# Performance work log

Hardware: AMD Instinct MI355X
Metric: run time of the kernel (lower is better)

Reference implementation:

```python
import jax, jax.numpy as jnp
import numpy as np

K = 64        # top-k from init_kwargs
TAU = 1.0     # temperature at step=0: tau_start*(1-0) + tau_end*0


def setup_inputs() -> dict:
    key = jax.random.key(0)
    k1, k2 = jax.random.split(key)
    B, N = 2048, 8192
    logits = jax.random.normal(k1, (B, N), dtype=jnp.float32)
    # gumbels = -log(Exp(1)) == standard Gumbel noise
    gumbel_noise = jax.random.gumbel(k2, (B, N), dtype=jnp.float32)
    return {"logits": logits, "gumbel_noise": gumbel_noise}


def reference(logits, gumbel_noise):
    # training path of GumbelTopK (step=0 -> tau=TAU, hard=True)
    g = (logits + gumbel_noise) / TAU                       # [B, N]
    order = jnp.argsort(-g, axis=-1)                        # descending sort order
    sorted_g = jnp.take_along_axis(g, order, axis=-1)
    cumsum = jnp.cumsum(jax.nn.softmax(sorted_g, axis=-1), axis=-1)
    mask = (cumsum <= K).astype(sorted_g.dtype)             # NB: faithful to source (<= k)
    sorted_y = mask * jax.nn.softmax(sorted_g / TAU, axis=-1)
    # scatter back to original positions == gather by inverse permutation
    inv = jnp.argsort(order, axis=-1)
    y = jnp.take_along_axis(sorted_y, inv, axis=-1)         # [B, N]
    # hard straight-through: one-hot-k of y
    k = min(K, y.shape[-1])
    _, idx = jax.lax.top_k(y, k)                            # [B, k]
    rows = jnp.arange(y.shape[0])[:, None]
    y_hard = jnp.zeros_like(y).at[rows, idx].set(1.0)
    return jax.lax.stop_gradient(y_hard - y) + y
```

## Files before the change

kernel.cpp:

```cpp
#include <hip/hip_runtime.h>

constexpr int N = 8192;
constexpr int K = 64;
constexpr int THREADS = 256;
constexpr int EPT = N / THREADS;
constexpr int HIST_BINS = 2048;

__device__ __forceinline__ unsigned orderable(float f) {
    unsigned x = __float_as_uint(f);
    return (x & 0x80000000u) ? ~x : (x | 0x80000000u);
}

__global__ __launch_bounds__(THREADS)
void gumbel_topk_onehot(const float* __restrict__ logits,
                        const float* __restrict__ noise,
                        float* __restrict__ out)
{
    __shared__ unsigned u_sh[N];
    __shared__ unsigned hist[HIST_BINS];
    __shared__ unsigned part[THREADS];
    __shared__ unsigned sel_prefix, sel_kth, sel_cnt;

    const int tid = threadIdx.x;
    const long long row = blockIdx.x;
    const float4* lrow = (const float4*)(logits + row * (long long)N);
    const float4* nrow = (const float4*)(noise  + row * (long long)N);

#pragma unroll
    for (int i = 0; i < EPT / 4; ++i) {
        int idx = tid + i * THREADS;
        float4 a = lrow[idx];
        float4 b = nrow[idx];
        u_sh[4 * idx + 0] = orderable(a.x + b.x);
        u_sh[4 * idx + 1] = orderable(a.y + b.y);
        u_sh[4 * idx + 2] = orderable(a.z + b.z);
        u_sh[4 * idx + 3] = orderable(a.w + b.w);
    }

    unsigned prefix = 0;
    unsigned kth = K;

#pragma unroll
    for (int r = 0; r < 3; ++r) {
        const int shift = (r == 0) ? 21 : (r == 1) ? 10 : 0;
        const int bits  = (r == 2) ? 10 : 11;
        const unsigned nb = 1u << bits;

        __syncthreads();
        for (int i = tid; i < HIST_BINS; i += THREADS) hist[i] = 0;
        __syncthreads();

        for (int i = tid; i < N; i += THREADS) {
            unsigned u = u_sh[i];
            bool match = (r == 0) ? true : ((u >> (shift + bits)) == prefix);
            if (match) atomicAdd(&hist[(u >> shift) & (nb - 1u)], 1u);
        }
        __syncthreads();

        const int bpt = nb / THREADS;
        unsigned p = 0;
#pragma unroll
        for (int j = 0; j < 8; ++j)
            if (j < bpt) p += hist[tid * bpt + j];
        part[tid] = p;
        __syncthreads();

        for (int off = 1; off < THREADS; off <<= 1) {
            unsigned v = (tid + off < THREADS) ? part[tid + off] : 0u;
            __syncthreads();
            part[tid] += v;
            __syncthreads();
        }

        unsigned snext = (tid + 1 < THREADS) ? part[tid + 1] : 0u;
        if (part[tid] >= kth && snext < kth) {
            unsigned cum = snext;
            for (int j = bpt - 1; j >= 0; --j) {
                unsigned c = hist[tid * bpt + j];
                if (cum + c >= kth) {
                    sel_prefix = (prefix << bits) | (unsigned)(tid * bpt + j);
                    sel_kth = kth - cum;
                    sel_cnt = c;
                    break;
                }
                cum += c;
            }
        }
        __syncthreads();
        prefix = sel_prefix;
        kth = sel_kth;
    }

    const unsigned T = prefix;
    const unsigned take_eq = kth;
    const unsigned c_eq = sel_cnt;
    const bool fastpath = (take_eq == c_eq);

    float4* orow = (float4*)(out + row * (long long)N);
#pragma unroll
    for (int i = 0; i < EPT / 4; ++i) {
        int idx = tid + i * THREADS;
        unsigned u0 = u_sh[4 * idx + 0];
        unsigned u1 = u_sh[4 * idx + 1];
        unsigned u2 = u_sh[4 * idx + 2];
        unsigned u3 = u_sh[4 * idx + 3];
        float4 o;
        o.x = (u0 > T || (fastpath && u0 == T)) ? 1.0f : 0.0f;
        o.y = (u1 > T || (fastpath && u1 == T)) ? 1.0f : 0.0f;
        o.z = (u2 > T || (fastpath && u2 == T)) ? 1.0f : 0.0f;
        o.w = (u3 > T || (fastpath && u3 == T)) ? 1.0f : 0.0f;
        orow[idx] = o;
    }

    if (!fastpath) {
        __syncthreads();
        if (tid == 0) {
            unsigned c = 0;
            float* orowf = out + row * (long long)N;
            for (int i = 0; i < N; ++i) {
                if (u_sh[i] == T) {
                    orowf[i] = 1.0f;
                    if (++c == take_eq) break;
                }
            }
        }
    }
}

extern "C" void kernel_launch(void* const* d_in, const int* in_sizes, int n_in,
                              void* d_out, int out_size, void* d_ws, size_t ws_size,
                              hipStream_t stream) {
    const float* logits = (const float*)d_in[0];
    const float* noise  = (const float*)d_in[1];
    float* out = (float*)d_out;
    const int rows = in_sizes[0] / N;
    gumbel_topk_onehot<<<rows, THREADS, 0, stream>>>(logits, noise, out);
}
```

Measured before the change: 185.6 us.

## Keep row keys in registers and radix-select over a compacted candidate list

Each thread now keeps its 32 keys in registers instead of staging the whole 8192-element row in shared memory. Passes two and three of the radix select build their histograms from a compacted candidate buffer of the first-pass bin, not by rescanning all N keys. The block-wide Hillis-Steele scan with many barriers is replaced by wave shuffle reductions, and launch bounds request 4 blocks per CU. In exchange the kernel uses more registers, the candidate buffer has a capacity fallback, and the rare tie path recomputes keys from global memory.

```diff
diff --git a/kernel.cpp b/kernel.cpp
--- a/kernel.cpp
+++ b/kernel.cpp
@@ -3,128 +3,185 @@
 constexpr int N = 8192;
 constexpr int K = 64;
 constexpr int THREADS = 256;
+constexpr int WAVES = THREADS / 64;
 constexpr int EPT = N / THREADS;
-constexpr int HIST_BINS = 2048;
+constexpr int VEC = EPT / 4;
+constexpr int CAP = 3072;
 
 __device__ __forceinline__ unsigned orderable(float f) {
     unsigned x = __float_as_uint(f);
     return (x & 0x80000000u) ? ~x : (x | 0x80000000u);
 }
 
-__global__ __launch_bounds__(THREADS)
+__global__ __launch_bounds__(THREADS, 4)
 void gumbel_topk_onehot(const float* __restrict__ logits,
                         const float* __restrict__ noise,
                         float* __restrict__ out)
 {
-    __shared__ unsigned u_sh[N];
-    __shared__ unsigned hist[HIST_BINS];
-    __shared__ unsigned part[THREADS];
-    __shared__ unsigned sel_prefix, sel_kth, sel_cnt;
+    __shared__ unsigned hist[2048];
+    __shared__ unsigned cand[CAP];
+    __shared__ unsigned wavesum[WAVES];
+    __shared__ unsigned ccount;
+    __shared__ unsigned sel_bin, sel_kth, sel_cnt;
 
-    const int tid = threadIdx.x;
+    const int tid  = threadIdx.x;
+    const int lane = tid & 63;
+    const int wave = tid >> 6;
     const long long row = blockIdx.x;
+
     const float4* lrow = (const float4*)(logits + row * (long long)N);
     const float4* nrow = (const float4*)(noise  + row * (long long)N);
 
+    unsigned key[EPT];
 #pragma unroll
-    for (int i = 0; i < EPT / 4; ++i) {
+    for (int i = 0; i < VEC; ++i) {
         int idx = tid + i * THREADS;
         float4 a = lrow[idx];
         float4 b = nrow[idx];
-        u_sh[4 * idx + 0] = orderable(a.x + b.x);
-        u_sh[4 * idx + 1] = orderable(a.y + b.y);
-        u_sh[4 * idx + 2] = orderable(a.z + b.z);
-        u_sh[4 * idx + 3] = orderable(a.w + b.w);
+        key[4*i+0] = orderable(a.x + b.x);
+        key[4*i+1] = orderable(a.y + b.y);
+        key[4*i+2] = orderable(a.z + b.z);
+        key[4*i+3] = orderable(a.w + b.w);
     }
 
-    unsigned prefix = 0;
+    {
+        uint4 z = make_uint4(0,0,0,0);
+        for (int i = tid; i < 512; i += THREADS) ((uint4*)hist)[i] = z;
+    }
+    if (tid == 0) ccount = 0;
+    __syncthreads();
+#pragma unroll
+    for (int e = 0; e < EPT; ++e)
+        atomicAdd(&hist[key[e] >> 21], 1u);
+    __syncthreads();
+
     unsigned kth = K;
 
-#pragma unroll
-    for (int r = 0; r < 3; ++r) {
-        const int shift = (r == 0) ? 21 : (r == 1) ? 10 : 0;
-        const int bits  = (r == 2) ? 10 : 11;
-        const unsigned nb = 1u << bits;
-
-        __syncthreads();
-        for (int i = tid; i < HIST_BINS; i += THREADS) hist[i] = 0;
-        __syncthreads();
-
-        for (int i = tid; i < N; i += THREADS) {
-            unsigned u = u_sh[i];
-            bool match = (r == 0) ? true : ((u >> (shift + bits)) == prefix);
-            if (match) atomicAdd(&hist[(u >> shift) & (nb - 1u)], 1u);
-        }
-        __syncthreads();
-
-        const int bpt = nb / THREADS;
-        unsigned p = 0;
-#pragma unroll
-        for (int j = 0; j < 8; ++j)
-            if (j < bpt) p += hist[tid * bpt + j];
-        part[tid] = p;
-        __syncthreads();
-
-        for (int off = 1; off < THREADS; off <<= 1) {
-            unsigned v = (tid + off < THREADS) ? part[tid + off] : 0u;
-            __syncthreads();
-            part[tid] += v;
-            __syncthreads();
-        }
-
-        unsigned snext = (tid + 1 < THREADS) ? part[tid + 1] : 0u;
-        if (part[tid] >= kth && snext < kth) {
-            unsigned cum = snext;
-            for (int j = bpt - 1; j >= 0; --j) {
-                unsigned c = hist[tid * bpt + j];
-                if (cum + c >= kth) {
-                    sel_prefix = (prefix << bits) | (unsigned)(tid * bpt + j);
-                    sel_kth = kth - cum;
-                    sel_cnt = c;
-                    break;
-                }
-                cum += c;
-            }
-        }
-        __syncthreads();
-        prefix = sel_prefix;
-        kth = sel_kth;
+#define SELECT_BIN(BPT)                                                      \
+    {                                                                        \
+        unsigned p = 0;                                                      \
+        _Pragma("unroll")                                                    \
+        for (int j = 0; j < (BPT); ++j) p += hist[tid * (BPT) + j];          \
+        unsigned s = p;                                                      \
+        _Pragma("unroll")                                                    \
+        for (int off = 1; off < 64; off <<= 1) {                             \
+            unsigned v = __shfl_down(s, off);                                \
+            if (lane + off < 64) s += v;                                     \
+        }                                                                    \
+        if (lane == 0) wavesum[wave] = s;                                    \
+        __syncthreads();                                                     \
+        unsigned S = s;                                                      \
+        _Pragma("unroll")                                                    \
+        for (int w = 0; w < WAVES; ++w) if (w > wave) S += wavesum[w];       \
+        unsigned Snext = S - p;                                              \
+        if (S >= kth && Snext < kth) {                                       \
+            unsigned cum = Snext;                                            \
+            for (int j = (BPT) - 1; j >= 0; --j) {                           \
+                unsigned c = hist[tid * (BPT) + j];                          \
+                if (cum + c >= kth) {                                        \
+                    sel_bin = (unsigned)(tid * (BPT) + j);                   \
+                    sel_kth = kth - cum;                                     \
+                    sel_cnt = c;                                             \
+                    break;                                                   \
+                }                                                            \
+                cum += c;                                                    \
+            }                                                                \
+        }                                                                    \
+        __syncthreads();                                                     \
     }
 
-    const unsigned T = prefix;
-    const unsigned take_eq = kth;
-    const unsigned c_eq = sel_cnt;
-    const bool fastpath = (take_eq == c_eq);
+    SELECT_BIN(8)
+    const unsigned b1   = sel_bin;
+    const unsigned cnt1 = sel_cnt;
+    kth = sel_kth;
+    __syncthreads();
+
+    const bool use_cand = (cnt1 <= (unsigned)CAP);
+#pragma unroll
+    for (int e = 0; e < EPT; ++e) {
+        if ((key[e] >> 21) == b1) {
+            unsigned pos = atomicAdd(&ccount, 1u);
+            if (pos < (unsigned)CAP) cand[pos] = key[e] & 0x1FFFFFu;
+        }
+    }
+
+    __syncthreads();
+    {
+        uint4 z = make_uint4(0,0,0,0);
+        for (int i = tid; i < 512; i += THREADS) ((uint4*)hist)[i] = z;
+    }
+    __syncthreads();
+    if (use_cand) {
+        for (int i = tid; i < (int)cnt1; i += THREADS)
+            atomicAdd(&hist[cand[i] >> 10], 1u);
+    } else {
+#pragma unroll
+        for (int e = 0; e < EPT; ++e)
+            if ((key[e] >> 21) == b1)
+                atomicAdd(&hist[(key[e] >> 10) & 0x7FFu], 1u);
+    }
+    __syncthreads();
+
+    SELECT_BIN(8)
+    const unsigned b2 = sel_bin;
+    kth = sel_kth;
+    __syncthreads();
+
+    {
+        uint4 z = make_uint4(0,0,0,0);
+        for (int i = tid; i < 256; i += THREADS) ((uint4*)hist)[i] = z;
+    }
+    __syncthreads();
+    if (use_cand) {
+        for (int i = tid; i < (int)cnt1; i += THREADS) {
+            unsigned cv = cand[i];
+            if ((cv >> 10) == b2) atomicAdd(&hist[cv & 0x3FFu], 1u);
+        }
+    } else {
+        const unsigned pfx = (b1 << 11) | b2;
+#pragma unroll
+        for (int e = 0; e < EPT; ++e)
+            if ((key[e] >> 10) == pfx)
+                atomicAdd(&hist[key[e] & 0x3FFu], 1u);
+    }
+    __syncthreads();
+
+    SELECT_BIN(4)
+    const unsigned b3      = sel_bin;
+    const unsigned take_eq = sel_kth;
+    const unsigned c_eq    = sel_cnt;
+
+    const unsigned T = (b1 << 21) | (b2 << 10) | b3;
+    const bool fast = (take_eq == c_eq);
 
     float4* orow = (float4*)(out + row * (long long)N);
 #pragma unroll
-    for (int i = 0; i < EPT / 4; ++i) {
+    for (int i = 0; i < VEC; ++i) {
         int idx = tid + i * THREADS;
-        unsigned u0 = u_sh[4 * idx + 0];
-        unsigned u1 = u_sh[4 * idx + 1];
-        unsigned u2 = u_sh[4 * idx + 2];
-        unsigned u3 = u_sh[4 * idx + 3];
         float4 o;
-        o.x = (u0 > T || (fastpath && u0 == T)) ? 1.0f : 0.0f;
-        o.y = (u1 > T || (fastpath && u1 == T)) ? 1.0f : 0.0f;
-        o.z = (u2 > T || (fastpath && u2 == T)) ? 1.0f : 0.0f;
-        o.w = (u3 > T || (fastpath && u3 == T)) ? 1.0f : 0.0f;
+        o.x = (key[4*i+0] > T || (fast && key[4*i+0] == T)) ? 1.0f : 0.0f;
+        o.y = (key[4*i+1] > T || (fast && key[4*i+1] == T)) ? 1.0f : 0.0f;
+        o.z = (key[4*i+2] > T || (fast && key[4*i+2] == T)) ? 1.0f : 0.0f;
+        o.w = (key[4*i+3] > T || (fast && key[4*i+3] == T)) ? 1.0f : 0.0f;
         orow[idx] = o;
     }
 
-    if (!fastpath) {
+    if (!fast) {
         __syncthreads();
         if (tid == 0) {
+            const float* lf = logits + row * (long long)N;
+            const float* nf = noise  + row * (long long)N;
+            float* of = out + row * (long long)N;
             unsigned c = 0;
-            float* orowf = out + row * (long long)N;
             for (int i = 0; i < N; ++i) {
-                if (u_sh[i] == T) {
-                    orowf[i] = 1.0f;
+                if (orderable(lf[i] + nf[i]) == T) {
+                    of[i] = 1.0f;
                     if (++c == take_eq) break;
                 }
             }
         }
     }
+#undef SELECT_BIN
 }
 
 extern "C" void kernel_launch(void* const* d_in, const int* in_sizes, int n_in,
```

Result: faster. 172.0 us (-7.3%).
